# Kernel tuning notes

Measured on AMD Instinct MI355X. Metric: run time of the kernel, lower is better.

Reference implementation:

```python
import jax, jax.numpy as jnp
import numpy as np

IN_F, OUT_F = 512, 512
GRID_SIZE, SPLINE_ORDER = 5, 3
K = GRID_SIZE + SPLINE_ORDER  # 8 basis functions
B, S = 8, 1024


def setup_inputs() -> dict:
    key = jax.random.key(0)
    k1, k2, k3, k4, k5 = jax.random.split(key, 5)
    return {
        "x": jax.random.normal(k1, (B, S, IN_F), dtype=jnp.float32),
        "coeff": jax.random.normal(k2, (OUT_F, IN_F, K), dtype=jnp.float32),
        "scale_base": jax.random.normal(k3, (OUT_F, IN_F), dtype=jnp.float32) * 0.1,
        "scale_spline": jax.random.normal(k4, (OUT_F, IN_F), dtype=jnp.float32),
        "base_bias": jax.random.normal(k5, (OUT_F, IN_F), dtype=jnp.float32),
    }


def reference(x, coeff, scale_base, scale_spline, base_bias):
    batch = x.shape[0]
    in_f = x.shape[-1]
    k = coeff.shape[-1]

    xc = jnp.clip(x.reshape(-1, in_f), -1.0, 1.0)      # (N, in)
    base = jax.nn.silu(xc)                              # (N, in)

    # polynomial basis recurrence: b0 = 1, b1 = x, b_i = 2*x*b_{i-1} - 1
    bases = [jnp.ones_like(xc), xc]
    for _ in range(2, k):
        bases.append(2.0 * xc * bases[-1] - 1.0)
    basis = jnp.stack(bases[:k], axis=-1)               # (N, in, K)

    # spline[n,o] = sum_{i,k} scale_spline[o,i]*coeff[o,i,k]*basis[n,i,k]
    w_spline = scale_spline[..., None] * coeff          # (out, in, K)
    spline_term = jnp.einsum('nik,oik->no', basis, w_spline)
    base_term = base @ scale_base.T                     # (N, out)
    out = base_term + spline_term + jnp.sum(base_bias, axis=1)  # (N, out)

    out = out.reshape(batch, -1, base_bias.shape[0])    # (B, S, out)
    if out.shape[-2] == 1:
        out = out[..., 0, :]
    return out
```

## Files before the change

kernel.cpp:

```cpp
#include <hip/hip_runtime.h>
#include <hip/hip_bf16.h>

#define IN_FEAT 512
#define OUT_FEAT 512
#define NTOK 8192
#define KDIM 4096

typedef short bf16x8 __attribute__((ext_vector_type(8)));
typedef float f32x16 __attribute__((ext_vector_type(16)));

static __device__ inline short f2bf(float f) {
    union { float f; unsigned u; } v; v.f = f;
    unsigned u = v.u;
    u += 0x7fffu + ((u >> 16) & 1u);
    return (short)(u >> 16);
}

static __device__ inline unsigned cvtpk(float lo, float hi) {
    unsigned r;
    asm("v_cvt_pk_bf16_f32 %0, %1, %2" : "=v"(r) : "v"(lo), "v"(hi));
    return r;
}

static __device__ inline bf16x8 gen_chunk(float xv) {
    float xc = fminf(fmaxf(xv, -1.f), 1.f);
    float e  = __expf(-xc);
    float bse = xc * __builtin_amdgcn_rcpf(1.f + e);
    float b2 = 2.f * xc * xc - 1.f;
    float b3 = 2.f * xc * b2 - 1.f;
    float b4 = 2.f * xc * b3 - 1.f;
    float b5 = 2.f * xc * b4 - 1.f;
    float b6 = 2.f * xc * b5 - 1.f;
    float b7 = 2.f * xc * b6 - 1.f;
    union { uint4 u; bf16x8 v; } r;
    r.u.x = cvtpk(bse, xc);
    r.u.y = cvtpk(b2, b3);
    r.u.z = cvtpk(b4, b5);
    r.u.w = cvtpk(b6, b7);
    return r.v;
}

static __device__ inline void gload_lds16(const short* g, short* l) {
    __builtin_amdgcn_global_load_lds(
        (const __attribute__((address_space(1))) unsigned int*)g,
        (__attribute__((address_space(3))) unsigned int*)l,
        16, 0, 0);
}

__global__ __launch_bounds__(256) void kan_prep(
    const float* __restrict__ coeff, const float* __restrict__ scale_base,
    const float* __restrict__ scale_spline, const float* __restrict__ base_bias,
    short* __restrict__ Wb, float* __restrict__ bias)
{
    int o = blockIdx.x;
    int tid = threadIdx.x;
    float local = 0.f;
#pragma unroll
    for (int rep = 0; rep < 2; ++rep) {
        int i = tid + rep * 256;
        size_t oi = (size_t)o * IN_FEAT + i;
        const float4* c4 = (const float4*)(coeff + oi * 8);
        float4 ca = c4[0], cb = c4[1];
        float ss = scale_spline[oi];
        float sb = scale_base[oi];
        local += base_bias[oi] + ss * ca.x;
        bf16x8 w;
        w[0] = f2bf(sb);
        w[1] = f2bf(ss * ca.y); w[2] = f2bf(ss * ca.z); w[3] = f2bf(ss * ca.w);
        w[4] = f2bf(ss * cb.x); w[5] = f2bf(ss * cb.y); w[6] = f2bf(ss * cb.z);
        w[7] = f2bf(ss * cb.w);
        *(bf16x8*)(Wb + (size_t)o * KDIM + (size_t)i * 8) = w;
    }
    __shared__ float red[4];
    for (int off = 32; off > 0; off >>= 1) local += __shfl_down(local, off, 64);
    int lane = tid & 63, wv = tid >> 6;
    if (lane == 0) red[wv] = local;
    __syncthreads();
    if (tid == 0) bias[o] = red[0] + red[1] + red[2] + red[3];
}

__global__ __launch_bounds__(256, 3) void kan_gemm15(
    const float* __restrict__ x, const short* __restrict__ Wb,
    const float* __restrict__ bias, float* __restrict__ out)
{
    __shared__ __align__(16) short POOL[24576];
    short* Bs = POOL;

    int tid = threadIdx.x;
    int nb = blockIdx.x & 7;
    int mb = blockIdx.x >> 3;
    int m0 = mb * 64, o0 = nb * 64;

    int lane = tid & 63, wv = tid >> 6;
    int kk = wv;
    int l31 = lane & 31, half = lane >> 5;
    int rm  = l31 & 15;

    f32x16 acc[2][2];
#pragma unroll
    for (int a = 0; a < 2; ++a)
#pragma unroll
        for (int b = 0; b < 2; ++b) acc[a][b] = (f32x16)0.f;

    int rl = lane >> 4, q = lane & 15;
    const short* pB0 = Wb + (size_t)(o0 + wv * 16 +  0 + rl) * KDIM + (size_t)(q ^ ( 0 + rl)) * 8;
    const short* pB1 = Wb + (size_t)(o0 + wv * 16 +  4 + rl) * KDIM + (size_t)(q ^ ( 4 + rl)) * 8;
    const short* pB2 = Wb + (size_t)(o0 + wv * 16 +  8 + rl) * KDIM + (size_t)(q ^ ( 8 + rl)) * 8;
    const short* pB3 = Wb + (size_t)(o0 + wv * 16 + 12 + rl) * KDIM + (size_t)(q ^ (12 + rl)) * 8;

    const float* xp0 = x + (size_t)(m0 + l31) * IN_FEAT + kk * 4;

    int s0 = kk * 4 + half, s1 = s0 + 2;
    int of00 = l31 * 128        + ((s0 ^ rm) * 8);
    int of01 = (32 + l31) * 128 + ((s0 ^ rm) * 8);
    int of10 = l31 * 128        + ((s1 ^ rm) * 8);
    int of11 = (32 + l31) * 128 + ((s1 ^ rm) * 8);

#define COMPUTE(CUR, P0, P1)                                                  \
    {                                                                         \
        const short* Bsc_ = Bs + (CUR) * 8192;                                \
        bf16x8 b00 = *(const bf16x8*)(Bsc_ + of00);                           \
        bf16x8 b01 = *(const bf16x8*)(Bsc_ + of01);                           \
        bf16x8 b10 = *(const bf16x8*)(Bsc_ + of10);                           \
        bf16x8 b11 = *(const bf16x8*)(Bsc_ + of11);                           \
        bf16x8 a00 = gen_chunk(half ? (P0).y : (P0).x);                       \
        bf16x8 a01 = gen_chunk(half ? (P1).y : (P1).x);                       \
        bf16x8 a10 = gen_chunk(half ? (P0).w : (P0).z);                       \
        bf16x8 a11 = gen_chunk(half ? (P1).w : (P1).z);                       \
        __builtin_amdgcn_s_setprio(1);                                        \
        acc[0][0] = __builtin_amdgcn_mfma_f32_32x32x16_bf16(a00, b00, acc[0][0], 0, 0, 0); \
        acc[0][1] = __builtin_amdgcn_mfma_f32_32x32x16_bf16(a00, b01, acc[0][1], 0, 0, 0); \
        acc[1][0] = __builtin_amdgcn_mfma_f32_32x32x16_bf16(a01, b00, acc[1][0], 0, 0, 0); \
        acc[1][1] = __builtin_amdgcn_mfma_f32_32x32x16_bf16(a01, b01, acc[1][1], 0, 0, 0); \
        acc[0][0] = __builtin_amdgcn_mfma_f32_32x32x16_bf16(a10, b10, acc[0][0], 0, 0, 0); \
        acc[0][1] = __builtin_amdgcn_mfma_f32_32x32x16_bf16(a10, b11, acc[0][1], 0, 0, 0); \
        acc[1][0] = __builtin_amdgcn_mfma_f32_32x32x16_bf16(a11, b10, acc[1][0], 0, 0, 0); \
        acc[1][1] = __builtin_amdgcn_mfma_f32_32x32x16_bf16(a11, b11, acc[1][1], 0, 0, 0); \
        __builtin_amdgcn_s_setprio(0);                                        \
    }

#define ISSUE_B(DST, IT)                                                      \
    {                                                                         \
        short* bd_ = Bs + (DST) * 8192 + wv * 2048;                           \
        const size_t bo_ = (size_t)(IT) * 128;                                \
        gload_lds16(pB0 + bo_, bd_);                                          \
        gload_lds16(pB1 + bo_, bd_ + 512);                                    \
        gload_lds16(pB2 + bo_, bd_ + 1024);                                   \
        gload_lds16(pB3 + bo_, bd_ + 1536);                                   \
    }

#define ITER(IT, CUR, DST, PC0, PC1, PN0, PN1)                                \
    {                                                                         \
        ISSUE_B(DST, (IT) + 2);                                               \
        {                                                                     \
            const float* xq_ = xp0 + (size_t)((IT) + 2) * 16;                 \
            PN0 = *(const float4*)(xq_);                                      \
            PN1 = *(const float4*)(xq_ + 16384);                              \
        }                                                                     \
        COMPUTE(CUR, PC0, PC1);                                               \
        asm volatile("s_waitcnt vmcnt(6)" ::: "memory");                      \
        __builtin_amdgcn_s_barrier();                                         \
    }

    float4 Pa0, Pa1, Pb0, Pb1, Pc0, Pc1;

    ISSUE_B(0, 0);
    Pa0 = *(const float4*)(xp0);
    Pa1 = *(const float4*)(xp0 + 16384);
    ISSUE_B(1, 1);
    Pb0 = *(const float4*)(xp0 + 16);
    Pb1 = *(const float4*)(xp0 + 16 + 16384);
    asm volatile("s_waitcnt vmcnt(6)" ::: "memory");
    __builtin_amdgcn_s_barrier();

    for (int j = 0; j < 10; ++j) {
        ITER(3 * j,     0, 2, Pa0, Pa1, Pc0, Pc1);
        ITER(3 * j + 1, 1, 0, Pb0, Pb1, Pa0, Pa1);
        ITER(3 * j + 2, 2, 1, Pc0, Pc1, Pb0, Pb1);
    }

    COMPUTE(0, Pa0, Pa1);
    asm volatile("s_waitcnt vmcnt(0)" ::: "memory");
    __builtin_amdgcn_s_barrier();
    COMPUTE(1, Pb0, Pb1);
#undef ITER
#undef ISSUE_B
#undef COMPUTE

    float* rbuf = (float*)POOL;
    __syncthreads();
    if (kk >= 2) {
        float* s_ = rbuf + (size_t)(kk - 2) * 4224 + lane * 66;
#pragma unroll
        for (int fm = 0; fm < 2; ++fm)
#pragma unroll
            for (int fn = 0; fn < 2; ++fn)
#pragma unroll
                for (int r = 0; r < 16; ++r)
                    s_[(fm * 2 + fn) * 16 + r] = acc[fm][fn][r];
    }
    __syncthreads();
    if (kk < 2) {
        const float* s_ = rbuf + (size_t)kk * 4224 + lane * 66;
#pragma unroll
        for (int fm = 0; fm < 2; ++fm)
#pragma unroll
            for (int fn = 0; fn < 2; ++fn)
#pragma unroll
                for (int r = 0; r < 16; ++r)
                    acc[fm][fn][r] += s_[(fm * 2 + fn) * 16 + r];
    }
    __syncthreads();
    if (kk == 1) {
        float* s_ = rbuf + lane * 66;
#pragma unroll
        for (int fm = 0; fm < 2; ++fm)
#pragma unroll
            for (int fn = 0; fn < 2; ++fn)
#pragma unroll
                for (int r = 0; r < 16; ++r)
                    s_[(fm * 2 + fn) * 16 + r] = acc[fm][fn][r];
    }
    __syncthreads();
    if (kk == 0) {
        const float* s_ = rbuf + lane * 66;
#pragma unroll
        for (int fn = 0; fn < 2; ++fn) {
            int o = o0 + fn * 32 + l31;
            float bv = bias[o];
#pragma unroll
            for (int fm = 0; fm < 2; ++fm) {
#pragma unroll
                for (int r = 0; r < 16; ++r) {
                    float v = acc[fm][fn][r] + s_[(fm * 2 + fn) * 16 + r] + bv;
                    int token = m0 + fm * 32 + (r & 3) + 8 * (r >> 2) + 4 * half;
                    out[(size_t)token * OUT_FEAT + o] = v;
                }
            }
        }
    }
}

extern "C" void kernel_launch(void* const* d_in, const int* in_sizes, int n_in,
                              void* d_out, int out_size, void* d_ws, size_t ws_size,
                              hipStream_t stream) {
    const float* x            = (const float*)d_in[0];
    const float* coeff        = (const float*)d_in[1];
    const float* scale_base   = (const float*)d_in[2];
    const float* scale_spline = (const float*)d_in[3];
    const float* base_bias    = (const float*)d_in[4];
    float* out = (float*)d_out;

    short* Wb   = (short*)d_ws;
    float* bias = (float*)((char*)d_ws + (size_t)OUT_FEAT * KDIM * 2);

    kan_prep<<<OUT_FEAT, 256, 0, stream>>>(coeff, scale_base, scale_spline, base_bias, Wb, bias);
    kan_gemm15<<<(NTOK / 64) * (OUT_FEAT / 64), 256, 0, stream>>>(x, Wb, bias, out);
}
```

Measured before the change: 135.9 us.

## Double M tile to 128 tokens and switch to double-buffered LDS pipeline

Each block now covers 128 tokens instead of 64, with 4x2 accumulators per wave, so each LDS-staged weight tile is reused across twice as many rows and grid size halves. The three-buffer vmcnt-counted pipeline is replaced by a two-buffer scheme with __syncthreads, and the x loads for four row groups are issued alongside the B loads. Occupancy drops from 3 to 2 blocks per CU because of the larger accumulator register footprint, and the simpler barrier scheme may expose more load latency. The epilogue reduction runs twice, once per half of the accumulators.

```diff
diff --git a/kernel.cpp b/kernel.cpp
--- a/kernel.cpp
+++ b/kernel.cpp
@@ -79,26 +79,26 @@
     if (tid == 0) bias[o] = red[0] + red[1] + red[2] + red[3];
 }
 
-__global__ __launch_bounds__(256, 3) void kan_gemm15(
+__global__ __launch_bounds__(256, 2) void kan_gemm16(
     const float* __restrict__ x, const short* __restrict__ Wb,
     const float* __restrict__ bias, float* __restrict__ out)
 {
-    __shared__ __align__(16) short POOL[24576];
+    __shared__ __align__(16) short POOL[20480];
     short* Bs = POOL;
 
     int tid = threadIdx.x;
     int nb = blockIdx.x & 7;
     int mb = blockIdx.x >> 3;
-    int m0 = mb * 64, o0 = nb * 64;
+    int m0 = mb * 128, o0 = nb * 64;
 
     int lane = tid & 63, wv = tid >> 6;
     int kk = wv;
     int l31 = lane & 31, half = lane >> 5;
     int rm  = l31 & 15;
 
-    f32x16 acc[2][2];
-#pragma unroll
-    for (int a = 0; a < 2; ++a)
+    f32x16 acc[4][2];
+#pragma unroll
+    for (int a = 0; a < 4; ++a)
 #pragma unroll
         for (int b = 0; b < 2; ++b) acc[a][b] = (f32x16)0.f;
 
@@ -116,125 +116,115 @@
     int of10 = l31 * 128        + ((s1 ^ rm) * 8);
     int of11 = (32 + l31) * 128 + ((s1 ^ rm) * 8);
 
-#define COMPUTE(CUR, P0, P1)                                                  \
+#define MFMA_(A, B, C) __builtin_amdgcn_mfma_f32_32x32x16_bf16(A, B, C, 0, 0, 0)
+
+#define STAGE(BUF, IT, P0, P1, P2, P3)                                        \
+    {                                                                         \
+        short* bd_ = Bs + (BUF) * 8192 + wv * 2048;                           \
+        const size_t bo_ = (size_t)(IT) * 128;                                \
+        gload_lds16(pB0 + bo_, bd_);                                          \
+        gload_lds16(pB1 + bo_, bd_ + 512);                                    \
+        gload_lds16(pB2 + bo_, bd_ + 1024);                                   \
+        gload_lds16(pB3 + bo_, bd_ + 1536);                                   \
+        const float* xq_ = xp0 + (size_t)(IT) * 16;                           \
+        P0 = *(const float4*)(xq_);                                           \
+        P1 = *(const float4*)(xq_ + 16384);                                   \
+        P2 = *(const float4*)(xq_ + 32768);                                   \
+        P3 = *(const float4*)(xq_ + 49152);                                   \
+    }
+
+#define COMPUTE(CUR, P0, P1, P2, P3)                                          \
     {                                                                         \
         const short* Bsc_ = Bs + (CUR) * 8192;                                \
         bf16x8 b00 = *(const bf16x8*)(Bsc_ + of00);                           \
         bf16x8 b01 = *(const bf16x8*)(Bsc_ + of01);                           \
         bf16x8 b10 = *(const bf16x8*)(Bsc_ + of10);                           \
         bf16x8 b11 = *(const bf16x8*)(Bsc_ + of11);                           \
-        bf16x8 a00 = gen_chunk(half ? (P0).y : (P0).x);                       \
-        bf16x8 a01 = gen_chunk(half ? (P1).y : (P1).x);                       \
-        bf16x8 a10 = gen_chunk(half ? (P0).w : (P0).z);                       \
-        bf16x8 a11 = gen_chunk(half ? (P1).w : (P1).z);                       \
-        __builtin_amdgcn_s_setprio(1);                                        \
-        acc[0][0] = __builtin_amdgcn_mfma_f32_32x32x16_bf16(a00, b00, acc[0][0], 0, 0, 0); \
-        acc[0][1] = __builtin_amdgcn_mfma_f32_32x32x16_bf16(a00, b01, acc[0][1], 0, 0, 0); \
-        acc[1][0] = __builtin_amdgcn_mfma_f32_32x32x16_bf16(a01, b00, acc[1][0], 0, 0, 0); \
-        acc[1][1] = __builtin_amdgcn_mfma_f32_32x32x16_bf16(a01, b01, acc[1][1], 0, 0, 0); \
-        acc[0][0] = __builtin_amdgcn_mfma_f32_32x32x16_bf16(a10, b10, acc[0][0], 0, 0, 0); \
-        acc[0][1] = __builtin_amdgcn_mfma_f32_32x32x16_bf16(a10, b11, acc[0][1], 0, 0, 0); \
-        acc[1][0] = __builtin_amdgcn_mfma_f32_32x32x16_bf16(a11, b10, acc[1][0], 0, 0, 0); \
-        acc[1][1] = __builtin_amdgcn_mfma_f32_32x32x16_bf16(a11, b11, acc[1][1], 0, 0, 0); \
-        __builtin_amdgcn_s_setprio(0);                                        \
-    }
-
-#define ISSUE_B(DST, IT)                                                      \
-    {                                                                         \
-        short* bd_ = Bs + (DST) * 8192 + wv * 2048;                           \
-        const size_t bo_ = (size_t)(IT) * 128;                                \
-        gload_lds16(pB0 + bo_, bd_);                                          \
-        gload_lds16(pB1 + bo_, bd_ + 512);                                    \
-        gload_lds16(pB2 + bo_, bd_ + 1024);                                   \
-        gload_lds16(pB3 + bo_, bd_ + 1536);                                   \
-    }
-
-#define ITER(IT, CUR, DST, PC0, PC1, PN0, PN1)                                \
-    {                                                                         \
-        ISSUE_B(DST, (IT) + 2);                                               \
-        {                                                                     \
-            const float* xq_ = xp0 + (size_t)((IT) + 2) * 16;                 \
-            PN0 = *(const float4*)(xq_);                                      \
-            PN1 = *(const float4*)(xq_ + 16384);                              \
-        }                                                                     \
-        COMPUTE(CUR, PC0, PC1);                                               \
-        asm volatile("s_waitcnt vmcnt(6)" ::: "memory");                      \
-        __builtin_amdgcn_s_barrier();                                         \
-    }
-
-    float4 Pa0, Pa1, Pb0, Pb1, Pc0, Pc1;
-
-    ISSUE_B(0, 0);
-    Pa0 = *(const float4*)(xp0);
-    Pa1 = *(const float4*)(xp0 + 16384);
-    ISSUE_B(1, 1);
-    Pb0 = *(const float4*)(xp0 + 16);
-    Pb1 = *(const float4*)(xp0 + 16 + 16384);
-    asm volatile("s_waitcnt vmcnt(6)" ::: "memory");
-    __builtin_amdgcn_s_barrier();
-
-    for (int j = 0; j < 10; ++j) {
-        ITER(3 * j,     0, 2, Pa0, Pa1, Pc0, Pc1);
-        ITER(3 * j + 1, 1, 0, Pb0, Pb1, Pa0, Pa1);
-        ITER(3 * j + 2, 2, 1, Pc0, Pc1, Pb0, Pb1);
-    }
-
-    COMPUTE(0, Pa0, Pa1);
-    asm volatile("s_waitcnt vmcnt(0)" ::: "memory");
-    __builtin_amdgcn_s_barrier();
-    COMPUTE(1, Pb0, Pb1);
-#undef ITER
-#undef ISSUE_B
+        bf16x8 a0 = gen_chunk(half ? (P0).y : (P0).x);                        \
+        bf16x8 a1 = gen_chunk(half ? (P1).y : (P1).x);                        \
+        bf16x8 a2 = gen_chunk(half ? (P2).y : (P2).x);                        \
+        bf16x8 a3 = gen_chunk(half ? (P3).y : (P3).x);                        \
+        acc[0][0] = MFMA_(a0, b00, acc[0][0]); acc[0][1] = MFMA_(a0, b01, acc[0][1]); \
+        acc[1][0] = MFMA_(a1, b00, acc[1][0]); acc[1][1] = MFMA_(a1, b01, acc[1][1]); \
+        acc[2][0] = MFMA_(a2, b00, acc[2][0]); acc[2][1] = MFMA_(a2, b01, acc[2][1]); \
+        acc[3][0] = MFMA_(a3, b00, acc[3][0]); acc[3][1] = MFMA_(a3, b01, acc[3][1]); \
+        a0 = gen_chunk(half ? (P0).w : (P0).z);                               \
+        a1 = gen_chunk(half ? (P1).w : (P1).z);                               \
+        a2 = gen_chunk(half ? (P2).w : (P2).z);                               \
+        a3 = gen_chunk(half ? (P3).w : (P3).z);                               \
+        acc[0][0] = MFMA_(a0, b10, acc[0][0]); acc[0][1] = MFMA_(a0, b11, acc[0][1]); \
+        acc[1][0] = MFMA_(a1, b10, acc[1][0]); acc[1][1] = MFMA_(a1, b11, acc[1][1]); \
+        acc[2][0] = MFMA_(a2, b10, acc[2][0]); acc[2][1] = MFMA_(a2, b11, acc[2][1]); \
+        acc[3][0] = MFMA_(a3, b10, acc[3][0]); acc[3][1] = MFMA_(a3, b11, acc[3][1]); \
+    }
+
+    float4 Pa0, Pa1, Pa2, Pa3, Pb0, Pb1, Pb2, Pb3;
+
+    STAGE(0, 0, Pa0, Pa1, Pa2, Pa3);
+    for (int j = 0; j < 16; ++j) {
+        const int e = 2 * j;
+        __syncthreads();
+        STAGE(1, e + 1, Pb0, Pb1, Pb2, Pb3);
+        COMPUTE(0, Pa0, Pa1, Pa2, Pa3);
+        __syncthreads();
+        if (e + 1 < 31) STAGE(0, e + 2, Pa0, Pa1, Pa2, Pa3);
+        COMPUTE(1, Pb0, Pb1, Pb2, Pb3);
+    }
+#undef STAGE
 #undef COMPUTE
+#undef MFMA_
 
     float* rbuf = (float*)POOL;
-    __syncthreads();
-    if (kk >= 2) {
-        float* s_ = rbuf + (size_t)(kk - 2) * 4224 + lane * 66;
-#pragma unroll
-        for (int fm = 0; fm < 2; ++fm)
-#pragma unroll
-            for (int fn = 0; fn < 2; ++fn)
-#pragma unroll
-                for (int r = 0; r < 16; ++r)
-                    s_[(fm * 2 + fn) * 16 + r] = acc[fm][fn][r];
-    }
-    __syncthreads();
-    if (kk < 2) {
-        const float* s_ = rbuf + (size_t)kk * 4224 + lane * 66;
-#pragma unroll
-        for (int fm = 0; fm < 2; ++fm)
-#pragma unroll
-            for (int fn = 0; fn < 2; ++fn)
-#pragma unroll
-                for (int r = 0; r < 16; ++r)
-                    acc[fm][fn][r] += s_[(fm * 2 + fn) * 16 + r];
-    }
-    __syncthreads();
-    if (kk == 1) {
-        float* s_ = rbuf + lane * 66;
-#pragma unroll
-        for (int fm = 0; fm < 2; ++fm)
-#pragma unroll
-            for (int fn = 0; fn < 2; ++fn)
-#pragma unroll
-                for (int r = 0; r < 16; ++r)
-                    s_[(fm * 2 + fn) * 16 + r] = acc[fm][fn][r];
-    }
-    __syncthreads();
-    if (kk == 0) {
-        const float* s_ = rbuf + lane * 66;
-#pragma unroll
-        for (int fn = 0; fn < 2; ++fn) {
-            int o = o0 + fn * 32 + l31;
-            float bv = bias[o];
-#pragma unroll
-            for (int fm = 0; fm < 2; ++fm) {
-#pragma unroll
-                for (int r = 0; r < 16; ++r) {
-                    float v = acc[fm][fn][r] + s_[(fm * 2 + fn) * 16 + r] + bv;
-                    int token = m0 + fm * 32 + (r & 3) + 8 * (r >> 2) + 4 * half;
-                    out[(size_t)token * OUT_FEAT + o] = v;
+#pragma unroll
+    for (int p = 0; p < 2; ++p) {
+        __syncthreads();
+        if (kk >= 2) {
+            float* s_ = rbuf + (size_t)(kk - 2) * 4224 + lane * 66;
+#pragma unroll
+            for (int fm = 0; fm < 2; ++fm)
+#pragma unroll
+                for (int fn = 0; fn < 2; ++fn)
+#pragma unroll
+                    for (int r = 0; r < 16; ++r)
+                        s_[(fm * 2 + fn) * 16 + r] = acc[2 * p + fm][fn][r];
+        }
+        __syncthreads();
+        if (kk < 2) {
+            const float* s_ = rbuf + (size_t)kk * 4224 + lane * 66;
+#pragma unroll
+            for (int fm = 0; fm < 2; ++fm)
+#pragma unroll
+                for (int fn = 0; fn < 2; ++fn)
+#pragma unroll
+                    for (int r = 0; r < 16; ++r)
+                        acc[2 * p + fm][fn][r] += s_[(fm * 2 + fn) * 16 + r];
+        }
+        __syncthreads();
+        if (kk == 1) {
+            float* s_ = rbuf + lane * 66;
+#pragma unroll
+            for (int fm = 0; fm < 2; ++fm)
+#pragma unroll
+                for (int fn = 0; fn < 2; ++fn)
+#pragma unroll
+                    for (int r = 0; r < 16; ++r)
+                        s_[(fm * 2 + fn) * 16 + r] = acc[2 * p + fm][fn][r];
+        }
+        __syncthreads();
+        if (kk == 0) {
+            const float* s_ = rbuf + lane * 66;
+#pragma unroll
+            for (int fn = 0; fn < 2; ++fn) {
+                int o = o0 + fn * 32 + l31;
+                float bv = bias[o];
+#pragma unroll
+                for (int fm = 0; fm < 2; ++fm) {
+#pragma unroll
+                    for (int r = 0; r < 16; ++r) {
+                        float v = acc[2 * p + fm][fn][r] + s_[(fm * 2 + fn) * 16 + r] + bv;
+                        int token = m0 + (2 * p + fm) * 32 + (r & 3) + 8 * (r >> 2) + 4 * half;
+                        out[(size_t)token * OUT_FEAT + o] = v;
+                    }
                 }
             }
         }
@@ -255,5 +245,5 @@
     float* bias = (float*)((char*)d_ws + (size_t)OUT_FEAT * KDIM * 2);
 
     kan_prep<<<OUT_FEAT, 256, 0, stream>>>(coeff, scale_base, scale_spline, base_bias, Wb, bias);
-    kan_gemm15<<<(NTOK / 64) * (OUT_FEAT / 64), 256, 0, stream>>>(x, Wb, bias, out);
-}
+    kan_gemm16<<<(NTOK / 128) * (OUT_FEAT / 64), 256, 0, stream>>>(x, Wb, bias, out);
+}
```

After: 127.9 us. 1.06x faster.
